# Performance work log

Hardware: AMD Instinct MI355X
Metric: run time of the kernel (lower is better)

## Reference

```python
import jax, jax.numpy as jnp
import numpy as np

B, S, HID = 1, 2048, 2048
NH, HD, BS = 16, 128, 64
RATIO = 0.5
THETA = 10000.0


def rotate_half(x):
    h = x.shape[-1] // 2
    return jnp.concatenate([-x[..., h:], x[..., :h]], axis=-1)


def setup_inputs() -> dict:
    key = jax.random.key(0)
    ks = jax.random.split(key, 6)
    return {
        "hidden_states": jax.random.normal(ks[0], (B, S, HID), jnp.float32),
        "q_w": jax.random.normal(ks[1], (HID, NH * HD), jnp.float32) * 0.02,
        "k_w": jax.random.normal(ks[2], (HID, NH * HD), jnp.float32) * 0.02,
        "v_w": jax.random.normal(ks[3], (HID, NH * HD), jnp.float32) * 0.02,
        "o_w": jax.random.normal(ks[4], (NH * HD, HID), jnp.float32) * 0.02,
        # nn.init.uniform_(-0.1, 0.1)
        "sparsity_pattern": jax.random.uniform(ks[5], (NH, S // BS, S // BS), jnp.float32, -0.1, 0.1),
    }


def reference(hidden_states, q_w, k_w, v_w, o_w, sparsity_pattern):
    b, s, _ = hidden_states.shape
    # QKV projections (torch Linear: x @ W.T; here weights stored as [in, out])
    q = (hidden_states @ q_w).reshape(b, s, NH, HD).transpose(0, 2, 1, 3)  # [b,h,s,d]
    k = (hidden_states @ k_w).reshape(b, s, NH, HD).transpose(0, 2, 1, 3)
    v = (hidden_states @ v_w).reshape(b, s, NH, HD).transpose(0, 2, 1, 3)

    # RoPE (position_ids = arange)
    inv_freq = 1.0 / (THETA ** (jnp.arange(0, HD, 2, dtype=jnp.float32) / HD))
    pos = jnp.arange(s, dtype=jnp.float32)
    freqs = pos[:, None] * inv_freq[None, :]           # [s, d/2]
    emb = jnp.concatenate([freqs, freqs], axis=-1)     # [s, d]
    cos = jnp.cos(emb)[None, None].astype(q.dtype)     # [1,1,s,d]
    sin = jnp.sin(emb)[None, None].astype(q.dtype)
    q = q * cos + rotate_half(q) * sin
    k = k * cos + rotate_half(k) * sin

    # Learned per-head block-sparse mask via per-head top-k threshold
    nqb = s // BS  # 32
    kk = max(1, int(NH * nqb * nqb * RATIO / NH))  # 512
    flat = sparsity_pattern.reshape(NH, -1)
    top_vals, _ = jax.lax.top_k(flat, kk)
    thresh = top_vals[:, -1][:, None, None]
    block_mask = (sparsity_pattern > thresh).astype(jnp.float32)  # [h, nqb, nkb]
    # expand block mask to token resolution: [h, s, s]
    mask_full = jnp.repeat(jnp.repeat(block_mask, BS, axis=1), BS, axis=2)

    # scores: selected blocks get QK^T/sqrt(d), unselected blocks are exactly 0
    scores = jnp.einsum('bhqd,bhkd->bhqk', q, k) / np.sqrt(HD).astype(np.float32)
    scores = scores * mask_full[None]

    probs = jax.nn.softmax(scores.astype(jnp.float32), axis=-1).astype(q.dtype)
    attn = jnp.einsum('bhqk,bhkd->bhqd', probs, v)
    attn = attn.transpose(0, 2, 1, 3).reshape(b, s, NH * HD)
    return attn @ o_w
```

## Files before the change

kernel.cpp:

```cpp
#include <hip/hip_runtime.h>
#include <hip/hip_bf16.h>
#include <cstdint>
#include <cstddef>

typedef __bf16 bf16x8 __attribute__((ext_vector_type(8)));
typedef float f32x4 __attribute__((ext_vector_type(4)));
typedef unsigned short u16;

#define SEQ 2048
#define NH 16
#define HD 128
#define DMODEL 2048
#define NQKV 6144
#define NB 32
#define KSEL 512

__device__ __forceinline__ u16 f2bf(float f) {
  unsigned u = __float_as_uint(f);
  u += 0x7fffu + ((u >> 16) & 1u);
  return (u16)(u >> 16);
}
__device__ __forceinline__ float bf2f(u16 b) {
  return __uint_as_float(((unsigned)b) << 16);
}

__device__ __forceinline__ void async_copy16(const void* g, void* l) {
  __builtin_amdgcn_global_load_lds(
      (__attribute__((address_space(1))) void*)(unsigned long long)g,
      (__attribute__((address_space(3))) void*)(unsigned)(unsigned long long)l,
      16, 0, 0);
}

__global__ __launch_bounds__(256) void pre_kernel(
    const float* __restrict__ hidden, const float* __restrict__ qw,
    const float* __restrict__ kw, const float* __restrict__ vw,
    const float* __restrict__ ow, const float* __restrict__ sp,
    u16* __restrict__ Xb, u16* __restrict__ Wqkvt, u16* __restrict__ Wot,
    int* __restrict__ sel_cnt, int* __restrict__ sel_idx, unsigned* __restrict__ sel_mask) {
  __shared__ __align__(16) char smem[64 * 65 * 4];
  int bid = blockIdx.x, t = threadIdx.x;
  if (bid < 16) {
    int h = bid;
    float* vals = (float*)smem;
    unsigned char* selb = (unsigned char*)(smem + 4096);
    for (int i = 0; i < 4; ++i) vals[t + i * 256] = sp[h * 1024 + t + i * 256];
    __syncthreads();
    for (int i = 0; i < 4; ++i) {
      float v = vals[t + i * 256];
      int cnt = 0;
      for (int j = 0; j < 1024; ++j) cnt += vals[j] > v ? 1 : 0;
      selb[t + i * 256] = (cnt < (KSEL - 1)) ? 1 : 0;
    }
    __syncthreads();
    if (t < NB) {
      int n = 0; unsigned m = 0;
      for (int kb = 0; kb < NB; ++kb) {
        if (selb[t * NB + kb]) { sel_idx[(h * NB + t) * NB + n] = kb; ++n; m |= 1u << kb; }
      }
      sel_cnt[h * NB + t] = n;
      sel_mask[h * NB + t] = m;
    }
    return;
  }
  if (bid < 1040) {
    int base = (bid - 16) * 1024 + t;
    float4 v0 = ((const float4*)hidden)[base];
    float4 v1 = ((const float4*)hidden)[base + 256];
    float4 v2 = ((const float4*)hidden)[base + 512];
    float4 v3 = ((const float4*)hidden)[base + 768];
    ((ushort4*)Xb)[base]       = make_ushort4(f2bf(v0.x), f2bf(v0.y), f2bf(v0.z), f2bf(v0.w));
    ((ushort4*)Xb)[base + 256] = make_ushort4(f2bf(v1.x), f2bf(v1.y), f2bf(v1.z), f2bf(v1.w));
    ((ushort4*)Xb)[base + 512] = make_ushort4(f2bf(v2.x), f2bf(v2.y), f2bf(v2.z), f2bf(v2.w));
    ((ushort4*)Xb)[base + 768] = make_ushort4(f2bf(v3.x), f2bf(v3.y), f2bf(v3.z), f2bf(v3.w));
    return;
  }
  float(*tile)[65] = (float(*)[65])smem;
  for (int ti = 0; ti < 2; ++ti) {
    int tidx = (bid - 1040) * 2 + ti;
    int wsel = tidx >> 10, rem = tidx & 1023, bx = rem & 31, by = rem >> 5;
    const float* in = (wsel == 0) ? qw : (wsel == 1) ? kw : (wsel == 2) ? vw : ow;
    u16* out = (wsel == 3) ? Wot : Wqkvt + (size_t)wsel * DMODEL * 2048;
    int c0 = bx * 64, r0 = by * 64;
    if (ti) __syncthreads();
#pragma unroll
    for (int i = 0; i < 4; ++i) {
      int chunk = i * 256 + t, r = chunk >> 4, c4 = chunk & 15;
      float4 v = *(const float4*)(in + (size_t)(r0 + r) * 2048 + c0 + c4 * 4);
      tile[r][c4 * 4 + 0] = v.x; tile[r][c4 * 4 + 1] = v.y;
      tile[r][c4 * 4 + 2] = v.z; tile[r][c4 * 4 + 3] = v.w;
    }
    __syncthreads();
#pragma unroll
    for (int i = 0; i < 4; ++i) {
      int item = i * 256 + t, cc = item >> 4, rr4 = item & 15;
      ushort4 o = make_ushort4(f2bf(tile[rr4 * 4 + 0][cc]), f2bf(tile[rr4 * 4 + 1][cc]),
                               f2bf(tile[rr4 * 4 + 2][cc]), f2bf(tile[rr4 * 4 + 3][cc]));
      *(ushort4*)(out + (size_t)(c0 + cc) * 2048 + r0 + rr4 * 4) = o;
    }
  }
}

template <int WRITE_BF16>
__global__ __launch_bounds__(256, 2) void gemm_bt_kernel(
    const u16* __restrict__ A, const u16* __restrict__ Bt, void* __restrict__ Cout,
    int M, int N, int K) {
  __shared__ __align__(16) u16 As[8192];
  __shared__ __align__(16) u16 Bs[8192];
  const int t = threadIdx.x;
  const int lane = t & 63, w = t >> 6;
  const int wm = (w >> 1) * 64, wn = (w & 1) * 64;
  const int quad = lane >> 4, l16 = lane & 15;
  const int m0 = blockIdx.y * 128, n0 = blockIdx.x * 128;

  f32x4 acc[4][4] = {};

  for (int kt = 0; kt < K; kt += 64) {
    __syncthreads();
#pragma unroll
    for (int j = 0; j < 4; ++j) {
      int sl = w * 256 + j * 64 + lane;
      int row = sl >> 3, c = (sl & 7) ^ (row & 7);
      const u16* ga = A + (size_t)(m0 + row) * K + kt + c * 8;
      const u16* gb = Bt + (size_t)(n0 + row) * K + kt + c * 8;
      async_copy16(ga, &As[(size_t)(w * 256 + j * 64) * 8]);
      async_copy16(gb, &Bs[(size_t)(w * 256 + j * 64) * 8]);
    }
    __syncthreads();
#pragma unroll
    for (int ks = 0; ks < 2; ++ks) {
      bf16x8 af[4], bfr[4];
#pragma unroll
      for (int mt = 0; mt < 4; ++mt) {
        int row = wm + mt * 16 + l16;
        af[mt] = *(const bf16x8*)(&As[(row * 8 + ((ks * 4 + quad) ^ (l16 & 7))) * 8]);
      }
#pragma unroll
      for (int nt = 0; nt < 4; ++nt) {
        int row = wn + nt * 16 + l16;
        bfr[nt] = *(const bf16x8*)(&Bs[(row * 8 + ((ks * 4 + quad) ^ (l16 & 7))) * 8]);
      }
#pragma unroll
      for (int mt = 0; mt < 4; ++mt)
#pragma unroll
        for (int nt = 0; nt < 4; ++nt)
          acc[mt][nt] = __builtin_amdgcn_mfma_f32_16x16x32_bf16(af[mt], bfr[nt], acc[mt][nt], 0, 0, 0);
    }
  }
#pragma unroll
  for (int mt = 0; mt < 4; ++mt)
#pragma unroll
    for (int nt = 0; nt < 4; ++nt)
#pragma unroll
      for (int p = 0; p < 4; ++p) {
        int row = m0 + wm + mt * 16 + quad * 4 + p;
        int col = n0 + wn + nt * 16 + l16;
        if (WRITE_BF16)
          ((u16*)Cout)[(size_t)row * N + col] = f2bf(acc[mt][nt][p]);
        else
          ((float*)Cout)[(size_t)row * N + col] = acc[mt][nt][p];
      }
}

__global__ __launch_bounds__(256, 2) void prep_kernel(
    const u16* __restrict__ QKVb, u16* __restrict__ Qh, u16* __restrict__ Kh,
    u16* __restrict__ Vt, float* __restrict__ Vbsum) {
  __shared__ float vtile[64][129];
  int sb = blockIdx.x, h = blockIdx.y;
  int s0 = sb * 64, t = threadIdx.x;
  int d = t & 127, rp = t >> 7;
  float inv_freq = powf(10000.0f, -(float)(2 * (d & 63)) / 128.0f);
  int dp = (d + 64) & 127;
  float sgn = (d < 64) ? -1.0f : 1.0f;
  for (int i = 0; i < 32; ++i) {
    int row = rp + i * 2;
    int s = s0 + row;
    const u16* base = QKVb + (size_t)s * NQKV + h * HD;
    float ang = (float)s * inv_freq;
    float cs = cosf(ang), sn = sinf(ang);
    float q = bf2f(base[d]), qp = bf2f(base[dp]);
    float k = bf2f(base[DMODEL + d]), kp = bf2f(base[DMODEL + dp]);
    Qh[((size_t)h * SEQ + s) * HD + d] = f2bf(q * cs + sgn * qp * sn);
    Kh[((size_t)h * SEQ + s) * HD + d] = f2bf(k * cs + sgn * kp * sn);
    vtile[row][d] = bf2f(base[2 * DMODEL + d]);
  }
  __syncthreads();
  int ss = t & 63, dg = t >> 6;
  for (int i = 0; i < 32; ++i) {
    int dd = dg + i * 4;
    Vt[((size_t)h * HD + dd) * SEQ + s0 + ss] = f2bf(vtile[ss][dd]);
  }
  if (t < HD) {
    float sum = 0.f;
    for (int r = 0; r < 64; ++r) sum += vtile[r][t];
    Vbsum[((size_t)h * NB + sb) * HD + t] = sum;
  }
}

__global__ __launch_bounds__(256, 2) void attn_kernel(
    const u16* __restrict__ Qh, const u16* __restrict__ Kh, const u16* __restrict__ Vt,
    const float* __restrict__ Vbsum, const int* __restrict__ sel_cnt,
    const int* __restrict__ sel_idx, const unsigned* __restrict__ sel_mask,
    u16* __restrict__ attnb) {
  __shared__ __align__(16) u16 Ks[2][8192];
  __shared__ __align__(16) u16 Vs[2][8192];
  __shared__ __align__(16) u16 pbuf[4][1024];
  int bid = blockIdx.x;
  int h = (bid & 7) * 2 + ((bid >> 3) >> 5);
  int qb = (bid >> 3) & 31;
  int t = threadIdx.x, lane = t & 63, w = t >> 6;
  int quad = lane >> 4, l16 = lane & 15;
  int rowblk = h * NB + qb;
  int nsel = sel_cnt[rowblk];
  unsigned smask = sel_mask[rowblk];
  const int* selrow = sel_idx + rowblk * NB;

  auto stageK = [&](int buf, int kb) {
    const u16* kbase = Kh + ((size_t)h * SEQ + kb * 64) * HD;
#pragma unroll
    for (int j = 0; j < 4; ++j) {
      int s = w * 256 + j * 64 + lane;
      int r = s >> 4, c = (s & 15) ^ (r & 15);
      async_copy16(kbase + (size_t)r * HD + c * 8, &Ks[buf][(w * 256 + j * 64) * 8]);
    }
  };
  auto stageV = [&](int buf, int kb) {
    const u16* vbase = Vt + (size_t)h * HD * SEQ + kb * 64;
#pragma unroll
    for (int j = 0; j < 4; ++j) {
      int s = w * 256 + j * 64 + lane;
      int d = s >> 3, c = (s & 7) ^ (d & 7);
      async_copy16(vbase + (size_t)d * SEQ + c * 8, &Vs[buf][(w * 256 + j * 64) * 8]);
    }
  };

  if (nsel > 0) { stageK(0, selrow[0]); stageV(0, selrow[0]); }

  float vc[8] = {};
  for (int kb = 0; kb < NB; ++kb)
    if (!((smask >> kb) & 1u)) {
      const float* vb = Vbsum + ((size_t)h * NB + kb) * HD + l16;
#pragma unroll
      for (int nt = 0; nt < 8; ++nt) vc[nt] += vb[nt * 16];
    }
  bf16x8 qf[4];
  {
    const u16* qbase = Qh + ((size_t)h * SEQ + qb * 64 + w * 16 + l16) * HD + quad * 8;
#pragma unroll
    for (int kk = 0; kk < 4; ++kk) qf[kk] = *(const bf16x8*)(qbase + kk * 32);
  }
  float rs[4] = {0.f, 0.f, 0.f, 0.f};
  f32x4 oacc[8] = {};
  const float scale = 0.08838834764831845f;
  u16* pb = pbuf[w];

  __syncthreads();

  for (int si = 0; si < nsel; ++si) {
    int cur = si & 1;
    if (si + 1 < nsel) {
      stageK(1 - cur, selrow[si + 1]);
      stageV(1 - cur, selrow[si + 1]);
    }

    f32x4 sacc[4] = {};
#pragma unroll
    for (int kk = 0; kk < 4; ++kk) {
#pragma unroll
      for (int nt = 0; nt < 4; ++nt) {
        int row = nt * 16 + l16;
        bf16x8 bfr = *(const bf16x8*)(&Ks[cur][(row * 16 + ((kk * 4 + quad) ^ l16)) * 8]);
        sacc[nt] = __builtin_amdgcn_mfma_f32_16x16x32_bf16(qf[kk], bfr, sacc[nt], 0, 0, 0);
      }
    }
#pragma unroll
    for (int nt = 0; nt < 4; ++nt) {
#pragma unroll
      for (int p = 0; p < 4; ++p) {
        float pv = __expf(sacc[nt][p] * scale);
        u16 pr = f2bf(pv);
        int row = quad * 4 + p, col = nt * 16 + l16;
        pb[row * 64 + (((col >> 3) ^ (row & 7)) << 3) + (col & 7)] = pr;
        rs[p] += bf2f(pr);
      }
    }
    asm volatile("s_waitcnt lgkmcnt(0)" ::: "memory");
#pragma unroll
    for (int ks2 = 0; ks2 < 2; ++ks2) {
      bf16x8 pf = *(const bf16x8*)(pb + l16 * 64 + (((ks2 * 4 + quad) ^ (l16 & 7)) << 3));
#pragma unroll
      for (int nt = 0; nt < 8; ++nt) {
        int d = nt * 16 + l16;
        bf16x8 vf = *(const bf16x8*)(&Vs[cur][(d * 8 + ((ks2 * 4 + quad) ^ (d & 7))) * 8]);
        oacc[nt] = __builtin_amdgcn_mfma_f32_16x16x32_bf16(pf, vf, oacc[nt], 0, 0, 0);
      }
    }
    __syncthreads();
  }
#pragma unroll
  for (int p = 0; p < 4; ++p)
#pragma unroll
    for (int off = 1; off < 16; off <<= 1)
      rs[p] += __shfl_xor(rs[p], off, 64);
  float cntm = (float)(64 * (NB - nsel));
#pragma unroll
  for (int p = 0; p < 4; ++p) {
    float inv = 1.0f / (rs[p] + cntm);
    int row = qb * 64 + w * 16 + quad * 4 + p;
#pragma unroll
    for (int nt = 0; nt < 8; ++nt) {
      float o = (oacc[nt][p] + vc[nt]) * inv;
      attnb[(size_t)row * DMODEL + h * HD + nt * 16 + l16] = f2bf(o);
    }
  }
}

extern "C" void kernel_launch(void* const* d_in, const int* in_sizes, int n_in,
                              void* d_out, int out_size, void* d_ws, size_t ws_size,
                              hipStream_t stream) {
  const float* hidden = (const float*)d_in[0];
  const float* q_w = (const float*)d_in[1];
  const float* k_w = (const float*)d_in[2];
  const float* v_w = (const float*)d_in[3];
  const float* o_w = (const float*)d_in[4];
  const float* sp  = (const float*)d_in[5];

  char* ws = (char*)d_ws;
  size_t off = 0;
  auto alloc = [&](size_t bytes) -> void* {
    void* p = ws + off;
    off += (bytes + 255) & ~(size_t)255;
    return p;
  };
  u16* Xb     = (u16*)alloc((size_t)SEQ * DMODEL * 2);
  u16* Wqkvt  = (u16*)alloc((size_t)NQKV * DMODEL * 2);
  u16* Wot    = (u16*)alloc((size_t)DMODEL * DMODEL * 2);
  u16* QKVb   = (u16*)alloc((size_t)SEQ * NQKV * 2);
  u16* Qh     = (u16*)alloc((size_t)NH * SEQ * HD * 2);
  u16* Kh     = (u16*)alloc((size_t)NH * SEQ * HD * 2);
  u16* Vt     = (u16*)alloc((size_t)NH * HD * SEQ * 2);
  float* Vbsum = (float*)alloc((size_t)NH * NB * HD * 4);
  int* sel_cnt = (int*)alloc(NH * NB * 4);
  int* sel_idx = (int*)alloc(NH * NB * NB * 4);
  unsigned* sel_mask = (unsigned*)alloc(NH * NB * 4);
  u16* attnb = Xb;

  pre_kernel<<<3088, 256, 0, stream>>>(hidden, q_w, k_w, v_w, o_w, sp,
                                       Xb, Wqkvt, Wot, sel_cnt, sel_idx, sel_mask);
  gemm_bt_kernel<1><<<dim3(NQKV / 128, SEQ / 128), 256, 0, stream>>>(
      Xb, Wqkvt, QKVb, SEQ, NQKV, DMODEL);
  prep_kernel<<<dim3(NB, NH), 256, 0, stream>>>(QKVb, Qh, Kh, Vt, Vbsum);
  attn_kernel<<<512, 256, 0, stream>>>(Qh, Kh, Vt, Vbsum, sel_cnt, sel_idx,
                                       sel_mask, attnb);
  gemm_bt_kernel<0><<<dim3(DMODEL / 128, SEQ / 128), 256, 0, stream>>>(
      attnb, Wot, d_out, SEQ, DMODEL, DMODEL);
}
```

Measured before the change: 289.4 us.

## Fuse RoPE and V transpose into QKV GEMM epilogue, split-K output GEMM

Removes the separate prep kernel and the bf16 QKV intermediate. The QKV GEMM epilogue now applies RoPE using a precomputed sin/cos table, writes Q/K per head, and writes V transposed along with per-block sums. To make this work, the column mapping per wave is remapped so each lane holds both halves of a rotation pair. The output projection uses split-K=2 with atomic float adds into a zeroed output, which adds a memset and atomic traffic but doubles the number of blocks for better CU occupancy.

```diff
diff --git a/kernel.cpp b/kernel.cpp
--- a/kernel.cpp
+++ b/kernel.cpp
@@ -36,7 +36,8 @@
     const float* __restrict__ kw, const float* __restrict__ vw,
     const float* __restrict__ ow, const float* __restrict__ sp,
     u16* __restrict__ Xb, u16* __restrict__ Wqkvt, u16* __restrict__ Wot,
-    int* __restrict__ sel_cnt, int* __restrict__ sel_idx, unsigned* __restrict__ sel_mask) {
+    int* __restrict__ sel_cnt, int* __restrict__ sel_idx, unsigned* __restrict__ sel_mask,
+    float2* __restrict__ sctab) {
   __shared__ __align__(16) char smem[64 * 65 * 4];
   int bid = blockIdx.x, t = threadIdx.x;
   if (bid < 16) {
@@ -62,8 +63,20 @@
     }
     return;
   }
-  if (bid < 1040) {
-    int base = (bid - 16) * 1024 + t;
+  if (bid < 32) {
+    int b = bid - 16;
+    for (int i = 0; i < 32; ++i) {
+      int idx = i * 256 + t;
+      int s = b * 128 + (idx >> 6), j = idx & 63;
+      float inv = powf(10000.0f, -(float)j / 64.0f);
+      float sn, cs;
+      sincosf((float)s * inv, &sn, &cs);
+      sctab[s * 64 + j] = make_float2(cs, sn);
+    }
+    return;
+  }
+  if (bid < 1056) {
+    int base = (bid - 32) * 1024 + t;
     float4 v0 = ((const float4*)hidden)[base];
     float4 v1 = ((const float4*)hidden)[base + 256];
     float4 v2 = ((const float4*)hidden)[base + 512];
@@ -76,7 +89,7 @@
   }
   float(*tile)[65] = (float(*)[65])smem;
   for (int ti = 0; ti < 2; ++ti) {
-    int tidx = (bid - 1040) * 2 + ti;
+    int tidx = (bid - 1056) * 2 + ti;
     int wsel = tidx >> 10, rem = tidx & 1023, bx = rem & 31, by = rem >> 5;
     const float* in = (wsel == 0) ? qw : (wsel == 1) ? kw : (wsel == 2) ? vw : ow;
     u16* out = (wsel == 3) ? Wot : Wqkvt + (size_t)wsel * DMODEL * 2048;
@@ -100,21 +113,24 @@
   }
 }
 
-template <int WRITE_BF16>
+template <int MODE>
 __global__ __launch_bounds__(256, 2) void gemm_bt_kernel(
     const u16* __restrict__ A, const u16* __restrict__ Bt, void* __restrict__ Cout,
-    int M, int N, int K) {
+    int M, int N, int K, const float2* __restrict__ sctab,
+    u16* __restrict__ Qh, u16* __restrict__ Kh, u16* __restrict__ Vt,
+    float* __restrict__ Vbsum) {
   __shared__ __align__(16) u16 As[8192];
   __shared__ __align__(16) u16 Bs[8192];
   const int t = threadIdx.x;
   const int lane = t & 63, w = t >> 6;
-  const int wm = (w >> 1) * 64, wn = (w & 1) * 64;
+  const int wm = (w >> 1) * 64;
   const int quad = lane >> 4, l16 = lane & 15;
   const int m0 = blockIdx.y * 128, n0 = blockIdx.x * 128;
+  const int ksplit = K / gridDim.z, kbeg = blockIdx.z * ksplit;
 
   f32x4 acc[4][4] = {};
 
-  for (int kt = 0; kt < K; kt += 64) {
+  for (int kt = kbeg; kt < kbeg + ksplit; kt += 64) {
     __syncthreads();
 #pragma unroll
     for (int j = 0; j < 4; ++j) {
@@ -136,7 +152,7 @@
       }
 #pragma unroll
       for (int nt = 0; nt < 4; ++nt) {
-        int row = wn + nt * 16 + l16;
+        int row = (w & 1) * 32 + (nt & 1) * 16 + (nt >> 1) * 64 + l16;
         bfr[nt] = *(const bf16x8*)(&Bs[(row * 8 + ((ks * 4 + quad) ^ (l16 & 7))) * 8]);
       }
 #pragma unroll
@@ -146,53 +162,63 @@
           acc[mt][nt] = __builtin_amdgcn_mfma_f32_16x16x32_bf16(af[mt], bfr[nt], acc[mt][nt], 0, 0, 0);
     }
   }
-#pragma unroll
-  for (int mt = 0; mt < 4; ++mt)
-#pragma unroll
-    for (int nt = 0; nt < 4; ++nt)
+  if (MODE < 2) {
+#pragma unroll
+    for (int mt = 0; mt < 4; ++mt)
+#pragma unroll
+      for (int nt = 0; nt < 4; ++nt) {
+        int coff = n0 + (w & 1) * 32 + (nt & 1) * 16 + (nt >> 1) * 64 + l16;
+#pragma unroll
+        for (int p = 0; p < 4; ++p) {
+          int row = m0 + wm + mt * 16 + quad * 4 + p;
+          if (MODE == 0)
+            ((float*)Cout)[(size_t)row * N + coff] = acc[mt][nt][p];
+          else
+            unsafeAtomicAdd(&((float*)Cout)[(size_t)row * N + coff], acc[mt][nt][p]);
+        }
+      }
+    return;
+  }
+  int wsel = n0 >> 11;
+  int h = (n0 >> 7) & 15;
+  if (wsel < 2) {
+    u16* dst = wsel ? Kh : Qh;
+#pragma unroll
+    for (int mt = 0; mt < 4; ++mt)
 #pragma unroll
       for (int p = 0; p < 4; ++p) {
-        int row = m0 + wm + mt * 16 + quad * 4 + p;
-        int col = n0 + wn + nt * 16 + l16;
-        if (WRITE_BF16)
-          ((u16*)Cout)[(size_t)row * N + col] = f2bf(acc[mt][nt][p]);
-        else
-          ((float*)Cout)[(size_t)row * N + col] = acc[mt][nt][p];
-      }
-}
-
-__global__ __launch_bounds__(256, 2) void prep_kernel(
-    const u16* __restrict__ QKVb, u16* __restrict__ Qh, u16* __restrict__ Kh,
-    u16* __restrict__ Vt, float* __restrict__ Vbsum) {
-  __shared__ float vtile[64][129];
-  int sb = blockIdx.x, h = blockIdx.y;
-  int s0 = sb * 64, t = threadIdx.x;
-  int d = t & 127, rp = t >> 7;
-  float inv_freq = powf(10000.0f, -(float)(2 * (d & 63)) / 128.0f);
-  int dp = (d + 64) & 127;
-  float sgn = (d < 64) ? -1.0f : 1.0f;
-  for (int i = 0; i < 32; ++i) {
-    int row = rp + i * 2;
-    int s = s0 + row;
-    const u16* base = QKVb + (size_t)s * NQKV + h * HD;
-    float ang = (float)s * inv_freq;
-    float cs = cosf(ang), sn = sinf(ang);
-    float q = bf2f(base[d]), qp = bf2f(base[dp]);
-    float k = bf2f(base[DMODEL + d]), kp = bf2f(base[DMODEL + dp]);
-    Qh[((size_t)h * SEQ + s) * HD + d] = f2bf(q * cs + sgn * qp * sn);
-    Kh[((size_t)h * SEQ + s) * HD + d] = f2bf(k * cs + sgn * kp * sn);
-    vtile[row][d] = bf2f(base[2 * DMODEL + d]);
-  }
-  __syncthreads();
-  int ss = t & 63, dg = t >> 6;
-  for (int i = 0; i < 32; ++i) {
-    int dd = dg + i * 4;
-    Vt[((size_t)h * HD + dd) * SEQ + s0 + ss] = f2bf(vtile[ss][dd]);
-  }
-  if (t < HD) {
-    float sum = 0.f;
-    for (int r = 0; r < 64; ++r) sum += vtile[r][t];
-    Vbsum[((size_t)h * NB + sb) * HD + t] = sum;
+        int s = m0 + wm + mt * 16 + quad * 4 + p;
+        const float2* trow = sctab + s * 64;
+        u16* drow = dst + ((size_t)h * SEQ + s) * HD;
+#pragma unroll
+        for (int nt = 0; nt < 2; ++nt) {
+          int j = (w & 1) * 32 + nt * 16 + l16;
+          float2 cs = trow[j];
+          float lo = acc[mt][nt][p], hi = acc[mt][nt + 2][p];
+          drow[j]      = f2bf(lo * cs.x - hi * cs.y);
+          drow[j + 64] = f2bf(hi * cs.x + lo * cs.y);
+        }
+      }
+  } else {
+    int sb = (m0 >> 6) + (wm >> 6);
+#pragma unroll
+    for (int nt = 0; nt < 4; ++nt) {
+      int d = (w & 1) * 32 + (nt & 1) * 16 + (nt >> 1) * 64 + l16;
+      u16* vrow = Vt + ((size_t)h * HD + d) * SEQ;
+      float bsum = 0.f;
+#pragma unroll
+      for (int mt = 0; mt < 4; ++mt)
+#pragma unroll
+        for (int p = 0; p < 4; ++p) {
+          int s = m0 + wm + mt * 16 + quad * 4 + p;
+          float v = acc[mt][nt][p];
+          vrow[s] = f2bf(v);
+          bsum += v;
+        }
+      bsum += __shfl_xor(bsum, 16, 64);
+      bsum += __shfl_xor(bsum, 32, 64);
+      if (quad == 0) Vbsum[((size_t)h * NB + sb) * HD + d] = bsum;
+    }
   }
 }
 
@@ -334,23 +360,24 @@
   u16* Xb     = (u16*)alloc((size_t)SEQ * DMODEL * 2);
   u16* Wqkvt  = (u16*)alloc((size_t)NQKV * DMODEL * 2);
   u16* Wot    = (u16*)alloc((size_t)DMODEL * DMODEL * 2);
-  u16* QKVb   = (u16*)alloc((size_t)SEQ * NQKV * 2);
   u16* Qh     = (u16*)alloc((size_t)NH * SEQ * HD * 2);
   u16* Kh     = (u16*)alloc((size_t)NH * SEQ * HD * 2);
   u16* Vt     = (u16*)alloc((size_t)NH * HD * SEQ * 2);
   float* Vbsum = (float*)alloc((size_t)NH * NB * HD * 4);
+  float2* sctab = (float2*)alloc((size_t)SEQ * 64 * 8);
   int* sel_cnt = (int*)alloc(NH * NB * 4);
   int* sel_idx = (int*)alloc(NH * NB * NB * 4);
   unsigned* sel_mask = (unsigned*)alloc(NH * NB * 4);
   u16* attnb = Xb;
 
-  pre_kernel<<<3088, 256, 0, stream>>>(hidden, q_w, k_w, v_w, o_w, sp,
-                                       Xb, Wqkvt, Wot, sel_cnt, sel_idx, sel_mask);
-  gemm_bt_kernel<1><<<dim3(NQKV / 128, SEQ / 128), 256, 0, stream>>>(
-      Xb, Wqkvt, QKVb, SEQ, NQKV, DMODEL);
-  prep_kernel<<<dim3(NB, NH), 256, 0, stream>>>(QKVb, Qh, Kh, Vt, Vbsum);
+  hipMemsetAsync(d_out, 0, (size_t)SEQ * DMODEL * 4, stream);
+
+  pre_kernel<<<3104, 256, 0, stream>>>(hidden, q_w, k_w, v_w, o_w, sp,
+                                       Xb, Wqkvt, Wot, sel_cnt, sel_idx, sel_mask, sctab);
+  gemm_bt_kernel<2><<<dim3(NQKV / 128, SEQ / 128, 1), 256, 0, stream>>>(
+      Xb, Wqkvt, nullptr, SEQ, NQKV, DMODEL, sctab, Qh, Kh, Vt, Vbsum);
   attn_kernel<<<512, 256, 0, stream>>>(Qh, Kh, Vt, Vbsum, sel_cnt, sel_idx,
                                        sel_mask, attnb);
-  gemm_bt_kernel<0><<<dim3(DMODEL / 128, SEQ / 128), 256, 0, stream>>>(
-      attnb, Wot, d_out, SEQ, DMODEL, DMODEL);
-}
+  gemm_bt_kernel<1><<<dim3(DMODEL / 128, SEQ / 128, 2), 256, 0, stream>>>(
+      attnb, Wot, d_out, SEQ, DMODEL, DMODEL, nullptr, nullptr, nullptr, nullptr, nullptr);
+}
```

Result: faster. 275.6 us (-4.8%).
